# Kernel optimization log

Hardware: AMD Instinct MI355X
Metric: run time of the kernel (lower is better)

The kernel has to match this reference:

```python
import jax, jax.numpy as jnp
import numpy as np

D_MODEL = 1024
HEADS = 16
D_K = D_MODEL // HEADS
THETA = 10000.0
NEG = -1.0e9


def _rope(t, offset=0):
    # t: [B, H, S, D]; standard interleaved rotary embedding, base THETA
    S, D = t.shape[-2], t.shape[-1]
    half = D // 2
    inv_freq = 1.0 / (THETA ** (jnp.arange(half, dtype=jnp.float32) * 2.0 / D))
    pos = jnp.arange(offset, offset + S, dtype=jnp.float32)
    ang = pos[:, None] * inv_freq[None, :]          # [S, half]
    cos, sin = jnp.cos(ang), jnp.sin(ang)
    t1, t2 = t[..., ::2], t[..., 1::2]              # even / odd lanes
    o1 = t1 * cos - t2 * sin
    o2 = t1 * sin + t2 * cos
    return jnp.stack([o1, o2], axis=-1).reshape(t.shape)


def setup_inputs() -> dict:
    key = jax.random.key(0)
    k0, k1, k2, k3, k4 = jax.random.split(key, 5)
    B, S = 2, 2048
    x = jax.random.normal(k0, (B, S, D_MODEL), dtype=jnp.float32)
    att_mask = jnp.ones((B, S), dtype=jnp.int32)
    scale = 0.02
    wq = jax.random.normal(k1, (D_MODEL, D_MODEL), dtype=jnp.float32) * scale
    wk = jax.random.normal(k2, (D_MODEL, D_MODEL), dtype=jnp.float32) * scale
    wv = jax.random.normal(k3, (D_MODEL, D_MODEL), dtype=jnp.float32) * scale
    wo = jax.random.normal(k4, (D_MODEL, D_MODEL), dtype=jnp.float32) * scale
    return {"x": x, "att_mask": att_mask, "wq": wq, "wk": wk, "wv": wv, "wo": wo}


def reference(x, att_mask, wq, wk, wv, wo):
    B, S, _ = x.shape
    # nn.Linear(bias=False): y = x @ W^T ; then split heads -> [B, H, S, d_k]
    q = (x @ wq.T).reshape(B, S, HEADS, D_K).transpose(0, 2, 1, 3)
    k = (x @ wk.T).reshape(B, S, HEADS, D_K).transpose(0, 2, 1, 3)
    v = (x @ wv.T).reshape(B, S, HEADS, D_K).transpose(0, 2, 1, 3)
    # use_rope=True, start_pos=0, use_cache=False path
    q = _rope(q)
    k = _rope(k)
    scores = jnp.einsum("bhqd,bhkd->bhqk", q, k) / np.sqrt(D_K).astype(np.float32)
    pad = (att_mask == 0)[:, None, None, :]          # [B,1,1,S]
    scores = jnp.where(pad, NEG, scores)
    causal = jnp.tril(jnp.ones((S, S), dtype=bool))  # [S, S]
    scores = jnp.where(causal, scores, NEG)
    att = jax.nn.softmax(scores, axis=-1)
    ctx = jnp.einsum("bhqk,bhkd->bhqd", att, v)      # [B,H,S,d_k]
    final = ctx.transpose(0, 2, 1, 3).reshape(B, S, HEADS * D_K)
    return final @ wo.T
```

## Files before the change

kernel.cpp:

```cpp
#include <hip/hip_runtime.h>
#include <hip/hip_bf16.h>
#include <cstdint>

typedef unsigned short u16;
typedef __bf16 bf16x8 __attribute__((ext_vector_type(8)));
typedef float f32x4 __attribute__((ext_vector_type(4)));

#define S_LEN 2048
#define NH 16
#define DK 64
#define DM 1024

__device__ __forceinline__ u16 f2bf(float f) {
  union { float f; uint32_t u; } c; c.f = f;
  uint32_t u = c.u;
  u += 0x7fffu + ((u >> 16) & 1u);
  return (u16)(u >> 16);
}

__device__ __forceinline__ void gl_lds16(const void* gsrc, void* ldst) {
  __builtin_amdgcn_global_load_lds(
      (const __attribute__((address_space(1))) unsigned int*)gsrc,
      (__attribute__((address_space(3))) unsigned int*)ldst,
      16, 0, 0);
}

#define MFMA16(a, b, c) __builtin_amdgcn_mfma_f32_16x16x32_bf16((a), (b), (c), 0, 0, 0)
#define VMW(N) asm volatile("s_waitcnt vmcnt(" #N ")" ::: "memory")
#define BARM() asm volatile("s_barrier" ::: "memory")

__global__ __launch_bounds__(256) void prep_all(
    const float* x, const float* wq, const float* wk, const float* wv, const float* wo,
    const int* amask,
    u16* xb, u16* wqb, u16* wkb, u16* wvb, u16* wob, float2* tab, int* mflag)
{
  const int bid = blockIdx.x;
  if (bid < 2048) {
#pragma unroll
    for (int it = 0; it < 4; ++it) {
      size_t i = ((size_t)bid * 256 + threadIdx.x) * 4 + (size_t)it * 2097152u;
      const float* src; u16* dst; size_t off;
      if (i < 4194304u)      { src = x;  dst = xb;  off = i; }
      else if (i < 5242880u) { src = wq; dst = wqb; off = i - 4194304u; }
      else if (i < 6291456u) { src = wk; dst = wkb; off = i - 5242880u; }
      else if (i < 7340032u) { src = wv; dst = wvb; off = i - 6291456u; }
      else                   { src = wo; dst = wob; off = i - 7340032u; }
      float4 v = *(const float4*)(src + off);
      ushort4 o;
      o.x = f2bf(v.x); o.y = f2bf(v.y); o.z = f2bf(v.z); o.w = f2bf(v.w);
      *(ushort4*)(dst + off) = o;
    }
  } else if (bid < 2304) {
    int i = (bid - 2048) * 256 + threadIdx.x;
    int pos = i >> 5, f = i & 31;
    float inv = powf(10000.0f, -(float)f / 32.0f);
    float ang = (float)pos * inv;
    tab[i] = make_float2(cosf(ang), sinf(ang));
  } else {
    const int f = bid - 2304;
    if (threadIdx.x < 64) {
      const int b = f >> 5, t = f & 31;
      int v = amask[b * S_LEN + t * 64 + threadIdx.x];
      int all = (int)__all(v != 0);
      if (threadIdx.x == 0) mflag[f] = all;
    }
  }
}

__global__ __launch_bounds__(256, 4) void gemm_qkv32(
    const u16* xb, const u16* wqb, const u16* wkb, const u16* wvb,
    const float2* tab, u16* Qr, u16* Kr, u16* Vt)
{
  __shared__ __align__(16) u16 ldsA[2][128 * 32];
  __shared__ __align__(16) u16 ldsB[2][128 * 32];

  const int bid = blockIdx.x;
  const int xcd = bid & 7, v = bid >> 3;
  const int m0 = (xcd * 4 + (v & 3)) * 128;
  const int nc = v >> 2;
  const int z = nc >> 3;
  const int n0z = (nc & 7) * 128;
  const u16* Wz = (z == 0) ? wqb : ((z == 1) ? wkb : wvb);

  const int tid = threadIdx.x;
  const int w = tid >> 6, lane = tid & 63;
  const int l15 = lane & 15, g = lane >> 4;
  const int wm = (w >> 1) * 64, wn = (w & 1) * 64;
  const int lr4 = lane >> 2;
  const int scolb = ((lane & 3) * 16) ^ ((lr4 & 3) << 4);

  f32x4 acc[4][4] = {};

  auto stage = [&](int buf, int kt) {
#pragma unroll
    for (int c = 0; c < 2; ++c) {
      const int rb = c * 64 + w * 16;
      const int row = rb + lr4;
      gl_lds16((const char*)(xb + (size_t)(m0 + row) * DM + kt) + scolb,
               (char*)&ldsA[buf][0] + rb * 64);
      gl_lds16((const char*)(Wz + (size_t)(n0z + row) * DM + kt) + scolb,
               (char*)&ldsB[buf][0] + rb * 64);
    }
  };

  stage(0, 0);
  int cur = 0;
  for (int kt = 0; kt < DM; kt += 32) {
    if (kt + 32 < DM) { stage(cur ^ 1, kt + 32); VMW(4); } else { VMW(0); }
    BARM();
    bf16x8 af[4], bfr[4];
#pragma unroll
    for (int i = 0; i < 4; ++i) {
      const int ar = wm + i * 16 + l15;
      af[i] = *(const bf16x8*)((const char*)&ldsA[cur][0] + ar * 64 +
                               ((g * 16) ^ ((ar & 3) << 4)));
      const int br = wn + i * 16 + l15;
      bfr[i] = *(const bf16x8*)((const char*)&ldsB[cur][0] + br * 64 +
                                ((g * 16) ^ ((br & 3) << 4)));
    }
    __builtin_amdgcn_s_setprio(1);
#pragma unroll
    for (int i = 0; i < 4; ++i)
#pragma unroll
      for (int j = 0; j < 4; ++j)
        acc[i][j] = MFMA16(af[i], bfr[j], acc[i][j]);
    __builtin_amdgcn_s_setprio(0);
    BARM();
    cur ^= 1;
  }

  u16* dst = (z == 0) ? Qr : Kr;
#pragma unroll
  for (int i = 0; i < 4; ++i) {
#pragma unroll
    for (int j = 0; j < 4; ++j) {
      const int n = n0z + wn + j * 16 + l15;
      const int h = n >> 6, d = n & 63;
#pragma unroll
      for (int r = 0; r < 4; ++r) {
        const int m = m0 + wm + i * 16 + g * 4 + r;
        const int b = m >> 11, s = m & 2047;
        float vv = acc[i][j][r];
        if (z < 2) {
          float p = __shfl_xor(vv, 1);
          float2 cs = tab[s * 32 + (d >> 1)];
          float o = vv * cs.x + ((d & 1) ? p : -p) * cs.y;
          if (z == 0) o *= 0.18033688011f;
          dst[((size_t)(b * NH + h) * S_LEN + s) * DK + d] = f2bf(o);
        } else {
          Vt[((size_t)(b * NH + h) * DK + d) * S_LEN + s] = f2bf(vv);
        }
      }
    }
  }
}

__global__ __launch_bounds__(256, 4) void gemm_out64(const u16* ctx, const u16* wob, float* out) {
  __shared__ __align__(16) u16 ldsA[2][128 * 32];
  __shared__ __align__(16) u16 ldsB[2][64 * 32];

  const int bid = blockIdx.x;
  const int xcd = bid & 7, v = bid >> 3;
  const int m0 = (xcd * 4 + (v & 3)) * 128;
  const int n0 = (v >> 2) * 64;

  const int tid = threadIdx.x;
  const int w = tid >> 6, lane = tid & 63;
  const int l15 = lane & 15, g = lane >> 4;
  const int wm = (w >> 1) * 64, wn = (w & 1) * 32;
  const int lr4 = lane >> 2;
  const int scolb = ((lane & 3) * 16) ^ ((lr4 & 3) << 4);

  f32x4 acc[4][2] = {};

  auto stage = [&](int buf, int kt) {
#pragma unroll
    for (int c = 0; c < 2; ++c) {
      const int rb = c * 64 + w * 16;
      const int row = rb + lr4;
      gl_lds16((const char*)(ctx + (size_t)(m0 + row) * DM + kt) + scolb,
               (char*)&ldsA[buf][0] + rb * 64);
    }
    const int rb = w * 16;
    const int row = rb + lr4;
    gl_lds16((const char*)(wob + (size_t)(n0 + row) * DM + kt) + scolb,
             (char*)&ldsB[buf][0] + rb * 64);
  };

  stage(0, 0);
  int cur = 0;
  for (int kt = 0; kt < DM; kt += 32) {
    if (kt + 32 < DM) { stage(cur ^ 1, kt + 32); VMW(3); } else { VMW(0); }
    BARM();
    bf16x8 af[4], bfr[2];
#pragma unroll
    for (int i = 0; i < 4; ++i) {
      const int ar = wm + i * 16 + l15;
      af[i] = *(const bf16x8*)((const char*)&ldsA[cur][0] + ar * 64 +
                               ((g * 16) ^ ((ar & 3) << 4)));
    }
#pragma unroll
    for (int j = 0; j < 2; ++j) {
      const int br = wn + j * 16 + l15;
      bfr[j] = *(const bf16x8*)((const char*)&ldsB[cur][0] + br * 64 +
                                ((g * 16) ^ ((br & 3) << 4)));
    }
    __builtin_amdgcn_s_setprio(1);
#pragma unroll
    for (int i = 0; i < 4; ++i)
#pragma unroll
      for (int j = 0; j < 2; ++j)
        acc[i][j] = MFMA16(af[i], bfr[j], acc[i][j]);
    __builtin_amdgcn_s_setprio(0);
    BARM();
    cur ^= 1;
  }

#pragma unroll
  for (int i = 0; i < 4; ++i)
#pragma unroll
    for (int j = 0; j < 2; ++j)
#pragma unroll
      for (int r = 0; r < 4; ++r)
        out[(size_t)(m0 + wm + i * 16 + g * 4 + r) * DM + n0 + wn + j * 16 + l15] = acc[i][j][r];
}

__global__ __launch_bounds__(256, 4) void attn15(
    const u16* Qr, const u16* Kr, const u16* Vt, const int* amask, const int* mflag,
    u16* ctx)
{
  __shared__ __align__(16) u16 ldsK[2][64 * 64];
  __shared__ __align__(16) u16 ldsV[2][64 * 64];
  __shared__ __align__(16) __bf16 plds[4][16 * 64];

  const int bh = blockIdx.x;
  const int band = 31 - blockIdx.y;
  const int b = bh >> 4, h = bh & 15;
  const int tid = threadIdx.x, w = tid >> 6, lane = tid & 63;
  const int l15 = lane & 15, g = lane >> 4;
  const int r8 = lane >> 3;
  const int sw = ((lane & 7) * 16) ^ (r8 << 4);

  const int q0 = band * 64 + w * 16;
  const int dTile = band;
  const int ntB = band + 1;

  const u16* Kb0 = Kr + (size_t)bh * S_LEN * DK;
  const u16* Vb0 = Vt + (size_t)bh * DK * S_LEN;
  const u16* Qb  = Qr + (size_t)bh * S_LEN * DK;

  bf16x8 qa0 = *(const bf16x8*)(Qb + (size_t)(q0 + l15) * DK + g * 8);
  bf16x8 qa1 = *(const bf16x8*)(Qb + (size_t)(q0 + l15) * DK + 32 + g * 8);

  union { u16 u[8]; bf16x8 v; } one_u;
#pragma unroll
  for (int i = 0; i < 8; ++i) one_u.u[i] = 0x3F80;
  const bf16x8 ones = one_u.v;

  float m[4];
  f32x4 lacc = {0.f, 0.f, 0.f, 0.f};
  f32x4 o[4];
#pragma unroll
  for (int r = 0; r < 4; ++r) m[r] = -3e38f;
#pragma unroll
  for (int dt = 0; dt < 4; ++dt) o[dt] = (f32x4){0.f, 0.f, 0.f, 0.f};

  auto stage = [&](int buf, int t) {
    const size_t kv0 = (size_t)t * 64;
#pragma unroll
    for (int c = 0; c < 2; ++c) {
      const int rb = w * 16 + c * 8;
      const int row = rb + r8;
      gl_lds16((const char*)(Kb0 + (kv0 + row) * DK) + sw,
               (char*)&ldsK[buf][0] + rb * 128);
      gl_lds16((const char*)(Vb0 + (size_t)row * S_LEN + kv0) + sw,
               (char*)&ldsV[buf][0] + rb * 128);
    }
  };

  stage(0, 0);
  int cur = 0;

  for (int t = 0; t < ntB; ++t) {
    if (t + 1 < ntB) { stage(cur ^ 1, t + 1); VMW(4); } else { VMW(0); }
    BARM();
    {
      const int kv0 = t * 64;
      const bool allok = mflag[(b << 5) + t] != 0;

      bf16x8 kb[4][2];
#pragma unroll
      for (int nt = 0; nt < 4; ++nt) {
        const int row = nt * 16 + l15;
#pragma unroll
        for (int ks = 0; ks < 2; ++ks)
          kb[nt][ks] = *(const bf16x8*)((const char*)&ldsK[cur][0] + row * 128 +
                                        ((ks * 64 + g * 16) ^ ((row & 7) << 4)));
      }
      f32x4 s[4];
#pragma unroll
      for (int nt = 0; nt < 4; ++nt) s[nt] = (f32x4){0.f, 0.f, 0.f, 0.f};
      __builtin_amdgcn_s_setprio(1);
#pragma unroll
      for (int nt = 0; nt < 4; ++nt) {
        s[nt] = MFMA16(qa0, kb[nt][0], s[nt]);
        s[nt] = MFMA16(qa1, kb[nt][1], s[nt]);
      }
      __builtin_amdgcn_s_setprio(0);

      if (!allok) {
#pragma unroll
        for (int nt = 0; nt < 4; ++nt) {
          const int pmv = amask[b * S_LEN + kv0 + nt * 16 + l15];
#pragma unroll
          for (int r = 0; r < 4; ++r)
            if (!pmv) s[nt][r] = -1e9f;
        }
      }
      if (t == dTile) {
#pragma unroll
        for (int nt = 0; nt < 4; ++nt) {
          const int kvc = kv0 + nt * 16 + l15;
#pragma unroll
          for (int r = 0; r < 4; ++r)
            s[nt][r] = (kvc <= q0 + g * 4 + r) ? s[nt][r] : -1e9f;
        }
      }

      float t4[4];
      bool grow = false;
#pragma unroll
      for (int r = 0; r < 4; ++r) {
        t4[r] = fmaxf(fmaxf(s[0][r], s[1][r]), fmaxf(s[2][r], s[3][r]));
        grow = grow || (t4[r] > m[r] + 11.5415603f);
      }
      if (__any((int)grow)) {
#pragma unroll
        for (int r = 0; r < 4; ++r) {
          float t0 = t4[r];
          t0 = fmaxf(t0, __shfl_xor(t0, 1));
          t0 = fmaxf(t0, __shfl_xor(t0, 2));
          t0 = fmaxf(t0, __shfl_xor(t0, 4));
          t0 = fmaxf(t0, __shfl_xor(t0, 8));
          const float mnew = fmaxf(m[r], t0);
          const float alpha = exp2f(m[r] - mnew);
          m[r] = mnew;
          lacc[r] *= alpha;
#pragma unroll
          for (int dt = 0; dt < 4; ++dt) o[dt][r] *= alpha;
        }
      }
      __bf16* pw = &plds[w][0];
#pragma unroll
      for (int r = 0; r < 4; ++r) {
        const int row = g * 4 + r;
#pragma unroll
        for (int nt = 0; nt < 4; ++nt)
          pw[row * 64 + ((nt * 16 + l15) ^ ((row & 7) << 3))] =
              (__bf16)exp2f(s[nt][r] - m[r]);
      }
      bf16x8 pa0 = *(const bf16x8*)(pw + l15 * 64 + ((g * 8) ^ ((l15 & 7) << 3)));
      bf16x8 pa1 = *(const bf16x8*)(pw + l15 * 64 + ((32 + g * 8) ^ ((l15 & 7) << 3)));
      bf16x8 vb[4][2];
#pragma unroll
      for (int dt = 0; dt < 4; ++dt) {
        const int row = dt * 16 + l15;
#pragma unroll
        for (int ks = 0; ks < 2; ++ks)
          vb[dt][ks] = *(const bf16x8*)((const char*)&ldsV[cur][0] + row * 128 +
                                        ((ks * 64 + g * 16) ^ ((row & 7) << 4)));
      }
      __builtin_amdgcn_s_setprio(1);
      lacc = MFMA16(pa0, ones, lacc);
      lacc = MFMA16(pa1, ones, lacc);
#pragma unroll
      for (int dt = 0; dt < 4; ++dt) {
        o[dt] = MFMA16(pa0, vb[dt][0], o[dt]);
        o[dt] = MFMA16(pa1, vb[dt][1], o[dt]);
      }
      __builtin_amdgcn_s_setprio(0);
    }
    BARM();
    cur ^= 1;
  }

#pragma unroll
  for (int dt = 0; dt < 4; ++dt)
#pragma unroll
    for (int r = 0; r < 4; ++r) {
      const int q = q0 + g * 4 + r;
      ctx[((size_t)(b * S_LEN + q)) * DM + h * DK + dt * 16 + l15] =
          f2bf(o[dt][r] / lacc[r]);
    }
}

extern "C" void kernel_launch(void* const* d_in, const int* in_sizes, int n_in,
                              void* d_out, int out_size, void* d_ws, size_t ws_size,
                              hipStream_t stream) {
  const float* x   = (const float*)d_in[0];
  const int* amask = (const int*)d_in[1];
  const float* wq  = (const float*)d_in[2];
  const float* wk  = (const float*)d_in[3];
  const float* wv  = (const float*)d_in[4];
  const float* wo  = (const float*)d_in[5];
  float* out = (float*)d_out;

  char* ws = (char*)d_ws;
  u16* xb    = (u16*)(ws);
  u16* wqb   = (u16*)(ws + ( 8u << 20));
  u16* wkb   = (u16*)(ws + (10u << 20));
  u16* wvb   = (u16*)(ws + (12u << 20));
  u16* wob   = (u16*)(ws + (14u << 20));
  float2* tab = (float2*)(ws + (16u << 20));
  int* mflag = (int*)(ws + (16u << 20) + (768u << 10));
  u16* Qr    = (u16*)(ws + (17u << 20));
  u16* Kr    = (u16*)(ws + (25u << 20));
  u16* Vt    = (u16*)(ws + (33u << 20));
  u16* ctx   = (u16*)(ws + (41u << 20));

  hipLaunchKernelGGL(prep_all, dim3(2368), dim3(256), 0, stream,
                     x, wq, wk, wv, wo, amask, xb, wqb, wkb, wvb, wob, tab, mflag);
  hipLaunchKernelGGL(gemm_qkv32, dim3(768), dim3(256), 0, stream,
                     xb, wqb, wkb, wvb, tab, Qr, Kr, Vt);
  hipLaunchKernelGGL(attn15, dim3(32, 32), dim3(256), 0, stream,
                     Qr, Kr, Vt, amask, mflag, ctx);
  hipLaunchKernelGGL(gemm_out64, dim3(512), dim3(256), 0, stream, ctx, wob, out);
}
```

Measured before the change: 125.4 us.

## Use 32-wide KV tiles with triple-buffered LDS and per-wave causal skip

The attention kernel now processes KV in 32-column tiles instead of 64, uses a three-deep LDS ring so the trailing barrier per iteration can be dropped, and lets each wave skip KV tiles entirely above its own diagonal. Smaller LDS footprint allows raising launch bounds to 5 blocks per CU. The intent is less wasted causal work, one fewer barrier per tile, and higher occupancy. In exchange there are twice as many loop iterations with more per-tile softmax overhead, and the single-barrier ring depends on the 3-buffer distance being sufficient for correctness.

```diff
diff --git a/kernel.cpp b/kernel.cpp
--- a/kernel.cpp
+++ b/kernel.cpp
@@ -225,13 +225,13 @@
         out[(size_t)(m0 + wm + i * 16 + g * 4 + r) * DM + n0 + wn + j * 16 + l15] = acc[i][j][r];
 }
 
-__global__ __launch_bounds__(256, 4) void attn15(
+__global__ __launch_bounds__(256, 5) void attn16(
     const u16* Qr, const u16* Kr, const u16* Vt, const int* amask, const int* mflag,
     u16* ctx)
 {
-  __shared__ __align__(16) u16 ldsK[2][64 * 64];
-  __shared__ __align__(16) u16 ldsV[2][64 * 64];
-  __shared__ __align__(16) __bf16 plds[4][16 * 64];
+  __shared__ __align__(16) u16 ldsK[3][32 * 64];
+  __shared__ __align__(16) u16 ldsV[3][64 * 32];
+  __shared__ __align__(16) __bf16 plds[4][16 * 32];
 
   const int bh = blockIdx.x;
   const int band = 31 - blockIdx.y;
@@ -239,11 +239,12 @@
   const int tid = threadIdx.x, w = tid >> 6, lane = tid & 63;
   const int l15 = lane & 15, g = lane >> 4;
   const int r8 = lane >> 3;
-  const int sw = ((lane & 7) * 16) ^ (r8 << 4);
+  const int swk = ((lane & 7) * 16) ^ ((r8 & 7) << 4);
+  const int swv = ((lane & 3) * 16) ^ (((lane >> 2) & 3) << 4);
 
   const int q0 = band * 64 + w * 16;
-  const int dTile = band;
-  const int ntB = band + 1;
+  const int dTile = band * 2 + (w >> 1);
+  const int ntB = band * 2 + 2;
 
   const u16* Kb0 = Kr + (size_t)bh * S_LEN * DK;
   const u16* Vb0 = Vt + (size_t)bh * DK * S_LEN;
@@ -266,43 +267,45 @@
   for (int dt = 0; dt < 4; ++dt) o[dt] = (f32x4){0.f, 0.f, 0.f, 0.f};
 
   auto stage = [&](int buf, int t) {
-    const size_t kv0 = (size_t)t * 64;
-#pragma unroll
-    for (int c = 0; c < 2; ++c) {
-      const int rb = w * 16 + c * 8;
-      const int row = rb + r8;
-      gl_lds16((const char*)(Kb0 + (kv0 + row) * DK) + sw,
-               (char*)&ldsK[buf][0] + rb * 128);
-      gl_lds16((const char*)(Vb0 + (size_t)row * S_LEN + kv0) + sw,
-               (char*)&ldsV[buf][0] + rb * 128);
-    }
+    const size_t kv0 = (size_t)t * 32;
+    const int krow = w * 8 + r8;
+    gl_lds16((const char*)(Kb0 + (kv0 + krow) * DK) + swk,
+             (char*)&ldsK[buf][0] + (w * 8) * 128);
+    const int vrow = w * 16 + (lane >> 2);
+    gl_lds16((const char*)(Vb0 + (size_t)vrow * S_LEN + kv0) + swv,
+             (char*)&ldsV[buf][0] + (w * 16) * 64);
   };
 
   stage(0, 0);
   int cur = 0;
 
   for (int t = 0; t < ntB; ++t) {
-    if (t + 1 < ntB) { stage(cur ^ 1, t + 1); VMW(4); } else { VMW(0); }
+    if (t + 1 < ntB) {
+      stage((cur + 1 == 3) ? 0 : cur + 1, t + 1);
+      VMW(2);
+    } else {
+      VMW(0);
+    }
     BARM();
-    {
-      const int kv0 = t * 64;
-      const bool allok = mflag[(b << 5) + t] != 0;
-
-      bf16x8 kb[4][2];
-#pragma unroll
-      for (int nt = 0; nt < 4; ++nt) {
+    if (t <= dTile) {
+      const int kv0 = t * 32;
+      const bool allok = mflag[(b << 5) + (t >> 1)] != 0;
+
+      bf16x8 kb[2][2];
+#pragma unroll
+      for (int nt = 0; nt < 2; ++nt) {
         const int row = nt * 16 + l15;
 #pragma unroll
         for (int ks = 0; ks < 2; ++ks)
           kb[nt][ks] = *(const bf16x8*)((const char*)&ldsK[cur][0] + row * 128 +
                                         ((ks * 64 + g * 16) ^ ((row & 7) << 4)));
       }
-      f32x4 s[4];
-#pragma unroll
-      for (int nt = 0; nt < 4; ++nt) s[nt] = (f32x4){0.f, 0.f, 0.f, 0.f};
+      f32x4 s[2];
+#pragma unroll
+      for (int nt = 0; nt < 2; ++nt) s[nt] = (f32x4){0.f, 0.f, 0.f, 0.f};
       __builtin_amdgcn_s_setprio(1);
 #pragma unroll
-      for (int nt = 0; nt < 4; ++nt) {
+      for (int nt = 0; nt < 2; ++nt) {
         s[nt] = MFMA16(qa0, kb[nt][0], s[nt]);
         s[nt] = MFMA16(qa1, kb[nt][1], s[nt]);
       }
@@ -310,7 +313,7 @@
 
       if (!allok) {
 #pragma unroll
-        for (int nt = 0; nt < 4; ++nt) {
+        for (int nt = 0; nt < 2; ++nt) {
           const int pmv = amask[b * S_LEN + kv0 + nt * 16 + l15];
 #pragma unroll
           for (int r = 0; r < 4; ++r)
@@ -319,7 +322,7 @@
       }
       if (t == dTile) {
 #pragma unroll
-        for (int nt = 0; nt < 4; ++nt) {
+        for (int nt = 0; nt < 2; ++nt) {
           const int kvc = kv0 + nt * 16 + l15;
 #pragma unroll
           for (int r = 0; r < 4; ++r)
@@ -331,7 +334,7 @@
       bool grow = false;
 #pragma unroll
       for (int r = 0; r < 4; ++r) {
-        t4[r] = fmaxf(fmaxf(s[0][r], s[1][r]), fmaxf(s[2][r], s[3][r]));
+        t4[r] = fmaxf(s[0][r], s[1][r]);
         grow = grow || (t4[r] > m[r] + 11.5415603f);
       }
       if (__any((int)grow)) {
@@ -355,33 +358,26 @@
       for (int r = 0; r < 4; ++r) {
         const int row = g * 4 + r;
 #pragma unroll
-        for (int nt = 0; nt < 4; ++nt)
-          pw[row * 64 + ((nt * 16 + l15) ^ ((row & 7) << 3))] =
+        for (int nt = 0; nt < 2; ++nt)
+          pw[row * 32 + ((nt * 16 + l15) ^ ((row & 3) << 3))] =
               (__bf16)exp2f(s[nt][r] - m[r]);
       }
-      bf16x8 pa0 = *(const bf16x8*)(pw + l15 * 64 + ((g * 8) ^ ((l15 & 7) << 3)));
-      bf16x8 pa1 = *(const bf16x8*)(pw + l15 * 64 + ((32 + g * 8) ^ ((l15 & 7) << 3)));
-      bf16x8 vb[4][2];
+      bf16x8 pa = *(const bf16x8*)(pw + l15 * 32 + ((g * 8) ^ ((l15 & 3) << 3)));
+      bf16x8 vb[4];
 #pragma unroll
       for (int dt = 0; dt < 4; ++dt) {
         const int row = dt * 16 + l15;
-#pragma unroll
-        for (int ks = 0; ks < 2; ++ks)
-          vb[dt][ks] = *(const bf16x8*)((const char*)&ldsV[cur][0] + row * 128 +
-                                        ((ks * 64 + g * 16) ^ ((row & 7) << 4)));
+        vb[dt] = *(const bf16x8*)((const char*)&ldsV[cur][0] + row * 64 +
+                                  ((g * 16) ^ ((row & 3) << 4)));
       }
       __builtin_amdgcn_s_setprio(1);
-      lacc = MFMA16(pa0, ones, lacc);
-      lacc = MFMA16(pa1, ones, lacc);
-#pragma unroll
-      for (int dt = 0; dt < 4; ++dt) {
-        o[dt] = MFMA16(pa0, vb[dt][0], o[dt]);
-        o[dt] = MFMA16(pa1, vb[dt][1], o[dt]);
-      }
+      lacc = MFMA16(pa, ones, lacc);
+#pragma unroll
+      for (int dt = 0; dt < 4; ++dt)
+        o[dt] = MFMA16(pa, vb[dt], o[dt]);
       __builtin_amdgcn_s_setprio(0);
     }
-    BARM();
-    cur ^= 1;
+    cur = (cur + 1 == 3) ? 0 : cur + 1;
   }
 
 #pragma unroll
@@ -422,7 +418,7 @@
                      x, wq, wk, wv, wo, amask, xb, wqb, wkb, wvb, wob, tab, mflag);
   hipLaunchKernelGGL(gemm_qkv32, dim3(768), dim3(256), 0, stream,
                      xb, wqb, wkb, wvb, tab, Qr, Kr, Vt);
-  hipLaunchKernelGGL(attn15, dim3(32, 32), dim3(256), 0, stream,
+  hipLaunchKernelGGL(attn16, dim3(32, 32), dim3(256), 0, stream,
                      Qr, Kr, Vt, amask, mflag, ctx);
   hipLaunchKernelGGL(gemm_out64, dim3(512), dim3(256), 0, stream, ctx, wob, out);
 }
```

Measured after the change: 137.3 us. 1.09x slower.
